# Optimization experiments

Measured on AMD Instinct MI355X. Metric: run time of the kernel, lower is better.

Reference implementation:

```python
import jax, jax.numpy as jnp
import numpy as np

BN_EPS = 1e-5


def setup_inputs() -> dict:
    key = jax.random.key(0)
    k_x, k_w, k_g, k_b, k_m, k_v = jax.random.split(key, 6)
    B, P, C = 8, 512, 1024
    x = jax.random.normal(k_x, (B, P, C), dtype=jnp.float32)
    # Linear(dim, dim, bias=False) weight, torch layout (out, in)
    W_qkv = jax.random.normal(k_w, (C, C), dtype=jnp.float32) * (1.0 / np.sqrt(C))
    # BatchNorm1d(dim) eval-mode params over channel axis
    bn_gamma = jnp.ones((C,), jnp.float32) + 0.01 * jax.random.normal(k_g, (C,), dtype=jnp.float32)
    bn_beta = 0.01 * jax.random.normal(k_b, (C,), dtype=jnp.float32)
    bn_mean = 0.01 * jax.random.normal(k_m, (C,), dtype=jnp.float32)
    bn_var = jnp.abs(1.0 + 0.01 * jax.random.normal(k_v, (C,), dtype=jnp.float32))
    gra_sharp = jnp.float32(2.0)
    return {"x": x, "W_qkv": W_qkv, "bn_gamma": bn_gamma, "bn_beta": bn_beta,
            "bn_mean": bn_mean, "bn_var": bn_var, "gra_sharp": gra_sharp}


def reference(x, W_qkv, bn_gamma, bn_beta, bn_mean, bn_var, gra_sharp):
    B, P, C = x.shape
    H = 8  # num_heads
    Wd = P // H  # per-head token width (heads split the SEQUENCE axis)

    # shared Linear(dim,dim,bias=False); q = k = v since same module on same x
    qkv = jnp.einsum('bpc,dc->bpd', x, W_qkv)          # (B, P, C)
    qkv = qkv.transpose(0, 2, 1)                        # (B, C, P)
    # BatchNorm1d(dim), eval mode: normalize channel axis (dim=1)
    inv = jax.lax.rsqrt(bn_var + BN_EPS)
    qkv = (qkv - bn_mean[None, :, None]) * (inv * bn_gamma)[None, :, None] + bn_beta[None, :, None]

    # split_last((H, -1)) on seq axis then transpose(1,2): (B, H, C, Wd)
    q = qkv.reshape(B, C, H, Wd).transpose(0, 2, 1, 3)
    k = q
    v = q

    # channel-by-channel scores per head: (B, H, C, C)
    scores = jnp.einsum('bhcw,bhdw->bhcd', q, k) / gra_sharp
    # NON-STANDARD: softmax over the HEAD axis (dim=1); dropout = identity (eval)
    attn = jax.nn.softmax(scores, axis=1)

    h = jnp.einsum('bhcd,bhdw->bhcw', attn, v)          # (B, H, C, Wd)
    h = h.transpose(0, 2, 1, 3).reshape(B, C, P)        # merge heads back into P
    h = h.transpose(0, 2, 1)                            # (B, P, C)
    return h, attn
```

## Files before the change

kernel.cpp:

```cpp
#include <hip/hip_runtime.h>
#include <math.h>

#define B 8
#define P 512
#define C 1024
#define H 8
#define BN_EPS 1e-5f

typedef __attribute__((ext_vector_type(8))) __bf16 bf16x8;
typedef __attribute__((ext_vector_type(4))) __bf16 bf16x4;
typedef __attribute__((ext_vector_type(4))) float f32x4;

__global__ __launch_bounds__(256) void split_hi_lo(
    const float* __restrict__ x, const float* __restrict__ Wq,
    __bf16* __restrict__ xhi, __bf16* __restrict__ xlo,
    __bf16* __restrict__ whi, __bf16* __restrict__ wlo)
{
    const size_t NX4 = (size_t)B * P * C / 4;
    size_t idx = (size_t)blockIdx.x * 256 + threadIdx.x;
    float4 v;
    __bf16 *dh, *dl;
    size_t o;
    if (idx < NX4) {
        v = ((const float4*)x)[idx];
        dh = xhi; dl = xlo; o = idx * 4;
    } else {
        v = ((const float4*)Wq)[idx - NX4];
        dh = whi; dl = wlo; o = (idx - NX4) * 4;
    }
    float f[4] = {v.x, v.y, v.z, v.w};
    bf16x4 hv, lv;
    #pragma unroll
    for (int j = 0; j < 4; ++j) {
        __bf16 hb = (__bf16)f[j];
        hv[j] = hb;
        lv[j] = (__bf16)(f[j] - (float)hb);
    }
    *(bf16x4*)&dh[o] = hv;
    *(bf16x4*)&dl[o] = lv;
}

__global__ __launch_bounds__(256) void qkv_bn_mfma(
    const __bf16* __restrict__ xhi, const __bf16* __restrict__ xlo,
    const __bf16* __restrict__ whi, const __bf16* __restrict__ wlo,
    const float* __restrict__ gamma, const float* __restrict__ beta,
    const float* __restrict__ mean, const float* __restrict__ var,
    __bf16* __restrict__ Yhi, __bf16* __restrict__ Ylo, __bf16* __restrict__ Zhi)
{
    const int dt = blockIdx.x;
    const int pt = blockIdx.y;
    const int b  = blockIdx.z;
    const int t = threadIdx.x, lane = t & 63, wid = t >> 6;
    const int quadd = (wid >> 1) * 32, quadp = (wid & 1) * 32;
    const int lr = lane & 15, lk = (lane >> 4) * 8;

    const int drow0 = dt * 64 + quadd + lr;
    const size_t xrow0 = ((size_t)b * P + pt * 64 + quadp + lr) * C;

    f32x4 acc[2][2];
    #pragma unroll
    for (int tm = 0; tm < 2; ++tm)
        #pragma unroll
        for (int tn = 0; tn < 2; ++tn)
            acc[tm][tn] = (f32x4){0.f, 0.f, 0.f, 0.f};

    for (int c0 = 0; c0 < C; c0 += 32) {
        const int col = c0 + lk;
        bf16x8 ah[2], al[2], bh[2], bl[2];
        #pragma unroll
        for (int tm = 0; tm < 2; ++tm) {
            size_t ia = (size_t)(drow0 + tm * 16) * C + col;
            ah[tm] = *(const bf16x8*)&whi[ia];
            al[tm] = *(const bf16x8*)&wlo[ia];
        }
        #pragma unroll
        for (int tn = 0; tn < 2; ++tn) {
            size_t ib = xrow0 + (size_t)tn * 16 * C + col;
            bh[tn] = *(const bf16x8*)&xhi[ib];
            bl[tn] = *(const bf16x8*)&xlo[ib];
        }
        #pragma unroll
        for (int tm = 0; tm < 2; ++tm)
            #pragma unroll
            for (int tn = 0; tn < 2; ++tn) {
                acc[tm][tn] = __builtin_amdgcn_mfma_f32_16x16x32_bf16(ah[tm], bh[tn], acc[tm][tn], 0, 0, 0);
                acc[tm][tn] = __builtin_amdgcn_mfma_f32_16x16x32_bf16(ah[tm], bl[tn], acc[tm][tn], 0, 0, 0);
                acc[tm][tn] = __builtin_amdgcn_mfma_f32_16x16x32_bf16(al[tm], bh[tn], acc[tm][tn], 0, 0, 0);
            }
    }

    const int rgrp = (lane >> 4) * 4;
    #pragma unroll
    for (int tm = 0; tm < 2; ++tm) {
        const int dbase = dt * 64 + quadd + tm * 16 + rgrp;
        float4 g4 = *(const float4*)&gamma[dbase];
        float4 bb4 = *(const float4*)&beta[dbase];
        float4 m4 = *(const float4*)&mean[dbase];
        float4 v4 = *(const float4*)&var[dbase];
        float gf[4] = {g4.x, g4.y, g4.z, g4.w};
        float bf[4] = {bb4.x, bb4.y, bb4.z, bb4.w};
        float mf[4] = {m4.x, m4.y, m4.z, m4.w};
        float vf[4] = {v4.x, v4.y, v4.z, v4.w};
        float sc[4];
        #pragma unroll
        for (int r = 0; r < 4; ++r) sc[r] = rsqrtf(vf[r] + BN_EPS) * gf[r];

        #pragma unroll
        for (int tn = 0; tn < 2; ++tn) {
            const int p = pt * 64 + quadp + tn * 16 + lr;
            bf16x4 zq;
            #pragma unroll
            for (int r = 0; r < 4; ++r) {
                float n = (acc[tm][tn][r] - mf[r]) * sc[r] + bf[r];
                __bf16 hb = (__bf16)n;
                __bf16 lb = (__bf16)(n - (float)hb);
                size_t yi = ((size_t)b * C + dbase + r) * P + p;
                Yhi[yi] = hb;
                Ylo[yi] = lb;
                zq[r] = hb;
            }
            *(bf16x4*)&Zhi[((size_t)b * P + p) * C + dbase] = zq;
        }
    }
}

__global__ __launch_bounds__(512) void attn_fused(
    const __bf16* __restrict__ Yhi, const __bf16* __restrict__ Ylo,
    const __bf16* __restrict__ Zhi, const float* __restrict__ gs_ptr,
    float* __restrict__ attn, float* __restrict__ out0)
{
    const int ct = blockIdx.x;
    const int b  = blockIdx.y;
    const int c0 = ct * 32;
    const int t = threadIdx.x, lane = t & 63, w = t >> 6;
    const int lr = lane & 15, lk = (lane >> 4) * 8, rgrp = (lane >> 4) * 4;
    const int si = w & 1;
    const int sq = w >> 1;
    const int pi = w & 1;
    const int pj = (w >> 1) & 1;
    const int pk = w >> 2;
    const float scale = 1.0f / gs_ptr[0];

    __shared__ __align__(16) char smem[65536];
    __bf16 (*Plds)[32][72] = (__bf16(*)[32][72])smem;
    float* Cmb = (float*)smem;
    float (*Olds)[36] = (float(*)[36])smem;

    f32x4 out_acc[8][2];
    #pragma unroll
    for (int h = 0; h < H; ++h) {
        out_acc[h][0] = (f32x4){0.f, 0.f, 0.f, 0.f};
        out_acc[h][1] = (f32x4){0.f, 0.f, 0.f, 0.f};
    }

    const int crow = c0 + si * 16 + lr;
    const size_t YbaseC = ((size_t)b * C + crow) * P;

    for (int dbase = 0; dbase < C; dbase += 64) {
        const int drow = dbase + sq * 16 + lr;
        const size_t YbaseD = ((size_t)b * C + drow) * P;

        f32x4 sacc[8];
        #pragma unroll
        for (int h = 0; h < H; ++h) sacc[h] = (f32x4){0.f, 0.f, 0.f, 0.f};

        #pragma unroll
        for (int h = 0; h < H; ++h) {
            #pragma unroll
            for (int s = 0; s < 2; ++s) {
                const int col = h * 64 + s * 32 + lk;
                bf16x8 ah = *(const bf16x8*)&Yhi[YbaseC + col];
                bf16x8 al = *(const bf16x8*)&Ylo[YbaseC + col];
                bf16x8 bh = *(const bf16x8*)&Yhi[YbaseD + col];
                bf16x8 bl = *(const bf16x8*)&Ylo[YbaseD + col];
                sacc[h] = __builtin_amdgcn_mfma_f32_16x16x32_bf16(ah, bh, sacc[h], 0, 0, 0);
                sacc[h] = __builtin_amdgcn_mfma_f32_16x16x32_bf16(ah, bl, sacc[h], 0, 0, 0);
                sacc[h] = __builtin_amdgcn_mfma_f32_16x16x32_bf16(al, bh, sacc[h], 0, 0, 0);
            }
        }

        const int dcol = dbase + sq * 16 + lr;
        #pragma unroll
        for (int r = 0; r < 4; ++r) {
            const int c = c0 + si * 16 + rgrp + r;
            float v[8];
            float m = -1e30f;
            #pragma unroll
            for (int h = 0; h < H; ++h) {
                v[h] = sacc[h][r] * scale;
                m = fmaxf(m, v[h]);
            }
            float ssum = 0.f;
            #pragma unroll
            for (int h = 0; h < H; ++h) { v[h] = __expf(v[h] - m); ssum += v[h]; }
            float inv = 1.0f / ssum;
            #pragma unroll
            for (int h = 0; h < H; ++h) {
                float p = v[h] * inv;
                attn[(((size_t)(b * H + h) * C + c) * C) + dcol] = p;
                Plds[h][si * 16 + rgrp + r][sq * 16 + lr] = (__bf16)p;
            }
        }
        __syncthreads();

        #pragma unroll
        for (int h = 0; h < H; ++h) {
            bf16x8 a = *(const bf16x8*)&Plds[h][pi * 16 + lr][pk * 32 + lk];
            #pragma unroll
            for (int tn = 0; tn < 2; ++tn) {
                const int p = h * 64 + pj * 32 + tn * 16 + lr;
                bf16x8 bv = *(const bf16x8*)&Zhi[((size_t)b * P + p) * C + dbase + pk * 32 + lk];
                out_acc[h][tn] = __builtin_amdgcn_mfma_f32_16x16x32_bf16(a, bv, out_acc[h][tn], 0, 0, 0);
            }
        }
        __syncthreads();
    }

    if (pk == 1) {
        float* reg = Cmb + (size_t)(w - 4) * 4096;
        #pragma unroll
        for (int h = 0; h < H; ++h)
            #pragma unroll
            for (int tn = 0; tn < 2; ++tn)
                #pragma unroll
                for (int r = 0; r < 4; ++r)
                    reg[((h * 2 + tn) * 4 + r) * 64 + lane] = out_acc[h][tn][r];
    }
    __syncthreads();
    if (pk == 0) {
        const float* reg = Cmb + (size_t)w * 4096;
        #pragma unroll
        for (int h = 0; h < H; ++h)
            #pragma unroll
            for (int tn = 0; tn < 2; ++tn)
                #pragma unroll
                for (int r = 0; r < 4; ++r)
                    out_acc[h][tn][r] += reg[((h * 2 + tn) * 4 + r) * 64 + lane];
    }
    __syncthreads();

    #pragma unroll
    for (int h = 0; h < H; ++h) {
        if (pk == 0) {
            #pragma unroll
            for (int tn = 0; tn < 2; ++tn)
                #pragma unroll
                for (int r = 0; r < 4; ++r)
                    Olds[pj * 32 + tn * 16 + lr][pi * 16 + rgrp + r] = out_acc[h][tn][r];
        }
        __syncthreads();
        {
            const int row = t >> 3;
            const int coff = (t & 7) * 4;
            f32x4 vv = *(const f32x4*)&Olds[row][coff];
            *(f32x4*)&out0[((size_t)b * P + h * 64 + row) * C + c0 + coff] = vv;
        }
        __syncthreads();
    }
}

extern "C" void kernel_launch(void* const* d_in, const int* in_sizes, int n_in,
                              void* d_out, int out_size, void* d_ws, size_t ws_size,
                              hipStream_t stream) {
    const float* x     = (const float*)d_in[0];
    const float* Wq    = (const float*)d_in[1];
    const float* gamma = (const float*)d_in[2];
    const float* beta  = (const float*)d_in[3];
    const float* mean  = (const float*)d_in[4];
    const float* var   = (const float*)d_in[5];
    const float* gs    = (const float*)d_in[6];

    float* out0 = (float*)d_out;
    float* attn = (float*)d_out + (size_t)B * P * C;

    const size_t NE = (size_t)B * C * P;
    __bf16* Yhi = (__bf16*)d_ws;
    __bf16* Ylo = Yhi + NE;
    __bf16* Zhi = Ylo + NE;

    const size_t attn_elems = (size_t)B * H * C * C;
    __bf16* S = (__bf16*)(attn + (attn_elems - 5242880));
    __bf16* xhi = S;
    __bf16* xlo = xhi + (size_t)B * P * C;
    __bf16* whi = xlo + (size_t)B * P * C;
    __bf16* wlo = whi + (size_t)C * C;

    split_hi_lo<<<5120, 256, 0, stream>>>(x, Wq, xhi, xlo, whi, wlo);
    qkv_bn_mfma<<<dim3(16, 8, 8), 256, 0, stream>>>(xhi, xlo, whi, wlo,
                                                    gamma, beta, mean, var,
                                                    Yhi, Ylo, Zhi);
    attn_fused<<<dim3(32, 8), 512, 0, stream>>>(Yhi, Ylo, Zhi, gs, attn, out0);
}
```

Baseline: 386.0 us.

## Shrink attention tiles to 16 rows, double grid, preload query hi fragments

The fused attention kernel now uses 16-channel row tiles with 256 threads per block and a 512-block 1D grid with batch interleaved, instead of 32-row tiles on 512 threads over 256 blocks. Each block's query-side hi fragments are loaded once into registers, and the split-K cross-wave reduction of the output accumulator is removed because each wave now owns a full K slice. The Zhi loads are issued before the barrier to overlap with the softmax stores. In exchange, each block re-reads the full d-side Y data for half as many rows, roughly doubling that global traffic, and register pressure rises from holding 16 preloaded fragments plus 16 prefetched B fragments.

```diff
diff --git a/kernel.cpp b/kernel.cpp
--- a/kernel.cpp
+++ b/kernel.cpp
@@ -124,40 +124,36 @@
     }
 }
 
-__global__ __launch_bounds__(512) void attn_fused(
+__global__ __launch_bounds__(256, 2) void attn_fused(
     const __bf16* __restrict__ Yhi, const __bf16* __restrict__ Ylo,
     const __bf16* __restrict__ Zhi, const float* __restrict__ gs_ptr,
     float* __restrict__ attn, float* __restrict__ out0)
 {
-    const int ct = blockIdx.x;
-    const int b  = blockIdx.y;
-    const int c0 = ct * 32;
+    const int id = blockIdx.x;
+    const int b  = id & 7;
+    const int ct = id >> 3;
+    const int c0 = ct * 16;
     const int t = threadIdx.x, lane = t & 63, w = t >> 6;
     const int lr = lane & 15, lk = (lane >> 4) * 8, rgrp = (lane >> 4) * 4;
-    const int si = w & 1;
-    const int sq = w >> 1;
-    const int pi = w & 1;
-    const int pj = (w >> 1) & 1;
-    const int pk = w >> 2;
     const float scale = 1.0f / gs_ptr[0];
 
-    __shared__ __align__(16) char smem[65536];
-    __bf16 (*Plds)[32][72] = (__bf16(*)[32][72])smem;
-    float* Cmb = (float*)smem;
-    float (*Olds)[36] = (float(*)[36])smem;
-
-    f32x4 out_acc[8][2];
-    #pragma unroll
-    for (int h = 0; h < H; ++h) {
-        out_acc[h][0] = (f32x4){0.f, 0.f, 0.f, 0.f};
-        out_acc[h][1] = (f32x4){0.f, 0.f, 0.f, 0.f};
-    }
-
-    const int crow = c0 + si * 16 + lr;
-    const size_t YbaseC = ((size_t)b * C + crow) * P;
+    __shared__ __bf16 Plds[8][16][72];
+    __shared__ float Olds[64][20];
+
+    const size_t YbaseC = ((size_t)b * C + c0 + lr) * P;
+    bf16x8 ah[16];
+    #pragma unroll
+    for (int h = 0; h < H; ++h)
+        #pragma unroll
+        for (int s = 0; s < 2; ++s)
+            ah[h * 2 + s] = *(const bf16x8*)&Yhi[YbaseC + h * 64 + s * 32 + lk];
+
+    f32x4 out_acc[8];
+    #pragma unroll
+    for (int h = 0; h < H; ++h) out_acc[h] = (f32x4){0.f, 0.f, 0.f, 0.f};
 
     for (int dbase = 0; dbase < C; dbase += 64) {
-        const int drow = dbase + sq * 16 + lr;
+        const int drow = dbase + w * 16 + lr;
         const size_t YbaseD = ((size_t)b * C + drow) * P;
 
         f32x4 sacc[8];
@@ -169,20 +165,19 @@
             #pragma unroll
             for (int s = 0; s < 2; ++s) {
                 const int col = h * 64 + s * 32 + lk;
-                bf16x8 ah = *(const bf16x8*)&Yhi[YbaseC + col];
-                bf16x8 al = *(const bf16x8*)&Ylo[YbaseC + col];
                 bf16x8 bh = *(const bf16x8*)&Yhi[YbaseD + col];
                 bf16x8 bl = *(const bf16x8*)&Ylo[YbaseD + col];
-                sacc[h] = __builtin_amdgcn_mfma_f32_16x16x32_bf16(ah, bh, sacc[h], 0, 0, 0);
-                sacc[h] = __builtin_amdgcn_mfma_f32_16x16x32_bf16(ah, bl, sacc[h], 0, 0, 0);
-                sacc[h] = __builtin_amdgcn_mfma_f32_16x16x32_bf16(al, bh, sacc[h], 0, 0, 0);
-            }
-        }
-
-        const int dcol = dbase + sq * 16 + lr;
+                bf16x8 av = *(const bf16x8*)&Ylo[YbaseC + col];
+                sacc[h] = __builtin_amdgcn_mfma_f32_16x16x32_bf16(ah[h * 2 + s], bh, sacc[h], 0, 0, 0);
+                sacc[h] = __builtin_amdgcn_mfma_f32_16x16x32_bf16(ah[h * 2 + s], bl, sacc[h], 0, 0, 0);
+                sacc[h] = __builtin_amdgcn_mfma_f32_16x16x32_bf16(av, bh, sacc[h], 0, 0, 0);
+            }
+        }
+
+        const int dcol = dbase + w * 16 + lr;
         #pragma unroll
         for (int r = 0; r < 4; ++r) {
-            const int c = c0 + si * 16 + rgrp + r;
+            const int c = c0 + rgrp + r;
             float v[8];
             float m = -1e30f;
             #pragma unroll
@@ -198,60 +193,40 @@
             for (int h = 0; h < H; ++h) {
                 float p = v[h] * inv;
                 attn[(((size_t)(b * H + h) * C + c) * C) + dcol] = p;
-                Plds[h][si * 16 + rgrp + r][sq * 16 + lr] = (__bf16)p;
-            }
-        }
-        __syncthreads();
-
+                Plds[h][rgrp + r][w * 16 + lr] = (__bf16)p;
+            }
+        }
+
+        bf16x8 bv[8][2];
         #pragma unroll
         for (int h = 0; h < H; ++h) {
-            bf16x8 a = *(const bf16x8*)&Plds[h][pi * 16 + lr][pk * 32 + lk];
-            #pragma unroll
-            for (int tn = 0; tn < 2; ++tn) {
-                const int p = h * 64 + pj * 32 + tn * 16 + lr;
-                bf16x8 bv = *(const bf16x8*)&Zhi[((size_t)b * P + p) * C + dbase + pk * 32 + lk];
-                out_acc[h][tn] = __builtin_amdgcn_mfma_f32_16x16x32_bf16(a, bv, out_acc[h][tn], 0, 0, 0);
-            }
-        }
-        __syncthreads();
-    }
-
-    if (pk == 1) {
-        float* reg = Cmb + (size_t)(w - 4) * 4096;
-        #pragma unroll
-        for (int h = 0; h < H; ++h)
-            #pragma unroll
-            for (int tn = 0; tn < 2; ++tn)
-                #pragma unroll
-                for (int r = 0; r < 4; ++r)
-                    reg[((h * 2 + tn) * 4 + r) * 64 + lane] = out_acc[h][tn][r];
-    }
-    __syncthreads();
-    if (pk == 0) {
-        const float* reg = Cmb + (size_t)w * 4096;
-        #pragma unroll
-        for (int h = 0; h < H; ++h)
-            #pragma unroll
-            for (int tn = 0; tn < 2; ++tn)
-                #pragma unroll
-                for (int r = 0; r < 4; ++r)
-                    out_acc[h][tn][r] += reg[((h * 2 + tn) * 4 + r) * 64 + lane];
-    }
-    __syncthreads();
+            const int p = h * 64 + w * 16 + lr;
+            #pragma unroll
+            for (int kh = 0; kh < 2; ++kh)
+                bv[h][kh] = *(const bf16x8*)&Zhi[((size_t)b * P + p) * C + dbase + kh * 32 + lk];
+        }
+        __syncthreads();
+
+        #pragma unroll
+        for (int h = 0; h < H; ++h) {
+            #pragma unroll
+            for (int kh = 0; kh < 2; ++kh) {
+                bf16x8 a = *(const bf16x8*)&Plds[h][lr][kh * 32 + lk];
+                out_acc[h] = __builtin_amdgcn_mfma_f32_16x16x32_bf16(a, bv[h][kh], out_acc[h], 0, 0, 0);
+            }
+        }
+        __syncthreads();
+    }
 
     #pragma unroll
     for (int h = 0; h < H; ++h) {
-        if (pk == 0) {
-            #pragma unroll
-            for (int tn = 0; tn < 2; ++tn)
-                #pragma unroll
-                for (int r = 0; r < 4; ++r)
-                    Olds[pj * 32 + tn * 16 + lr][pi * 16 + rgrp + r] = out_acc[h][tn][r];
-        }
+        #pragma unroll
+        for (int r = 0; r < 4; ++r)
+            Olds[w * 16 + lr][rgrp + r] = out_acc[h][r];
         __syncthreads();
         {
-            const int row = t >> 3;
-            const int coff = (t & 7) * 4;
+            const int row = t >> 2;
+            const int coff = (t & 3) * 4;
             f32x4 vv = *(const f32x4*)&Olds[row][coff];
             *(f32x4*)&out0[((size_t)b * P + h * 64 + row) * C + c0 + coff] = vv;
         }
@@ -289,5 +264,5 @@
     qkv_bn_mfma<<<dim3(16, 8, 8), 256, 0, stream>>>(xhi, xlo, whi, wlo,
                                                     gamma, beta, mean, var,
                                                     Yhi, Ylo, Zhi);
-    attn_fused<<<dim3(32, 8), 512, 0, stream>>>(Yhi, Ylo, Zhi, gs, attn, out0);
-}
+    attn_fused<<<512, 256, 0, stream>>>(Yhi, Ylo, Zhi, gs, attn, out0);
+}
```

Result: faster. 331.9 us (-14.0%).
